# Kernel optimization log

Measured on AMD Instinct MI355X. Metric: run time of the kernel, lower is better.

The kernel has to match this reference:

```python
import jax, jax.numpy as jnp
import numpy as np
from jax import lax


def setup_inputs() -> dict:
    key = jax.random.key(0)
    k1, k2 = jax.random.split(key)
    B, C, H, W = 4, 64, 64, 64
    foreground = jax.random.normal(k1, (B, C, H, W), dtype=jnp.float32)
    masks = jax.random.uniform(k2, (B, 1, H, W), dtype=jnp.float32)
    return {"foreground": foreground, "masks": masks}


def reference(foreground, masks):
    # First-call path of KnowledgeConsistentAttention (att_scores_prev is None).
    # patch_size=3 -> padding=1 around 1x1 dynamic kernels; propagate_size=3 -> 3x3 sum pool.
    B, C, H, W = foreground.shape
    P = H * W
    # Dynamic 1x1 kernels: one per spatial location, L2-normalized over channels.
    K = foreground.reshape(B, C, P).transpose(0, 2, 1)            # [B, P, C]
    norm = jnp.sqrt(jnp.sum(K * K, axis=2, keepdims=True))        # flatten(1).norm per kernel
    K = K / (norm + 1e-8)
    # conv2d with 1x1 kernels and padding=1 == GEMM over zero-padded input.
    Xpad = jnp.pad(foreground, ((0, 0), (0, 0), (1, 1), (1, 1)))  # [B, C, H+2, W+2]
    scores = jnp.einsum('bpc,bchw->bphw', K, Xpad)                # [B, P, H+2, W+2]
    # avg_pool2d(k=3, stride=1, pad=1) * 9 == zero-padded 3x3 sum pool.
    scores = lax.reduce_window(scores, jnp.float32(0.0), lax.add,
                               (1, 1, 3, 3), (1, 1, 1, 1), 'SAME')
    attn = jax.nn.softmax(scores, axis=1)                          # softmax over P kernels
    # conv_transpose2d with 1x1 kernels, padding=1 crops the border back to HxW.
    out = jnp.einsum('bphw,bpc->bchw', attn[:, :, 1:-1, 1:-1], K)  # [B, C, H, W]
    return out
```

## Files before the change

kernel.cpp:

```cpp
#include <hip/hip_runtime.h>
#include <hip/hip_bf16.h>
#include <math.h>

#define Bn 4
#define Cn 64
#define Pn 4096
#define QT 32
#define PBK 128
#define NITER (Pn / PBK)
#define LOG2E 1.4426950408889634f

typedef __attribute__((ext_vector_type(8))) short short8;
typedef __attribute__((ext_vector_type(4))) short short4v;
typedef __attribute__((ext_vector_type(4))) float float4v;
typedef unsigned short bfu;

__device__ __forceinline__ bfu f2bf(float x) {
    unsigned u = __float_as_uint(x);
    u = (u + 0x7fffu + ((u >> 16) & 1u)) >> 16;
    return (bfu)u;
}

__device__ __forceinline__ void async_load16(const bfu* g, bfu* l) {
    __builtin_amdgcn_global_load_lds(
        (const __attribute__((address_space(1))) unsigned int*)(const void*)g,
        (__attribute__((address_space(3))) unsigned int*)(void*)l,
        16, 0, 0);
}

__global__ __launch_bounds__(256) void prep_kernel(const float* __restrict__ fg,
                                                   bfu* __restrict__ Kpc,
                                                   bfu* __restrict__ Kcp2,
                                                   float* __restrict__ S) {
    __shared__ float shbuf[64 * 64];
    int t = threadIdx.x;
    if (blockIdx.x < 512) {
        float* tile  = shbuf;
        float* rnorm = shbuf + 64 * 33;
        int b  = blockIdx.x >> 7;
        int p0 = (blockIdx.x & 127) << 5;
        const float* src = fg + (size_t)b * Cn * Pn + p0;
        #pragma unroll
        for (int i = 0; i < 8; ++i) {
            int idx = i * 256 + t;
            int c = idx >> 5, p = idx & 31;
            tile[c * 33 + p] = src[(size_t)c * Pn + p];
        }
        __syncthreads();
        if (t < 32) {
            float ss = 0.f;
            #pragma unroll
            for (int c = 0; c < 64; ++c) { float v = tile[c * 33 + t]; ss += v * v; }
            rnorm[t] = 1.0f / (sqrtf(ss) + 1e-8f);
        }
        __syncthreads();
        bfu* dpc = Kpc + ((size_t)b * Pn + p0) * Cn;
        #pragma unroll
        for (int i = 0; i < 8; ++i) {
            int idx = i * 256 + t;
            int p = idx >> 6, c = idx & 63;
            dpc[(size_t)p * Cn + c] = f2bf(tile[c * 33 + p] * rnorm[p]);
        }
        bfu* d2 = Kcp2 + ((size_t)b * 256 + (p0 >> 4)) * 1024;
        #pragma unroll
        for (int i = 0; i < 8; ++i) {
            int idx = i * 256 + t;
            int c = idx >> 5, p = idx & 31;
            d2[(size_t)(p >> 4) * 1024 + c * 16 + (p & 15)] =
                f2bf(tile[c * 33 + p] * rnorm[p]);
        }
    } else {
        float (*pl)[64] = (float(*)[64])shbuf;
        int bc = blockIdx.x - 512;
        const float* src = fg + (size_t)bc * Pn;
        float*       dst = S  + (size_t)bc * Pn;
        #pragma unroll
        for (int i = 0; i < 16; ++i) {
            int idx = i * 256 + t;
            pl[idx >> 6][idx & 63] = src[idx];
        }
        __syncthreads();
        #pragma unroll
        for (int i = 0; i < 16; ++i) {
            int idx = i * 256 + t;
            int h = idx >> 6, w = idx & 63;
            float s = 0.f;
            #pragma unroll
            for (int dh = -1; dh <= 1; ++dh) {
                int hh = h + dh;
                if (hh < 0 || hh >= 64) continue;
                #pragma unroll
                for (int dw = -1; dw <= 1; ++dw) {
                    int ww = w + dw;
                    if (ww < 0 || ww >= 64) continue;
                    s += pl[hh][ww];
                }
            }
            dst[idx] = s * LOG2E;
        }
    }
}

__global__ __launch_bounds__(512, 4) void flash_kernel(const bfu* __restrict__ Kpc,
                                                       const bfu* __restrict__ Kcp2,
                                                       const float* __restrict__ S,
                                                       float* __restrict__ out) {
    __shared__ __align__(16) bfu smem[18432];
    __shared__ float wredl[8][QT];
    bfu* Sl = smem + 16384;

    int b  = blockIdx.x >> 7;
    int q0 = (blockIdx.x & 127) * QT;
    int t  = threadIdx.x;
    int w = t >> 6, l = t & 63, lq = l & 15, quad = l >> 4;

    const float* Sg  = S    + (size_t)b * Cn * Pn;
    const bfu*   gpc = Kpc  + (size_t)b * Pn * Cn;
    const bfu*   gt  = Kcp2 + (size_t)b * 256 * 1024;

    {
        int c = t >> 3, qq = (t & 7) * 4;
        const float* sp = &Sg[(size_t)c * Pn + q0 + qq];
        float4 v0 = *(const float4*)sp;
        float vv[4] = {v0.x, v0.y, v0.z, v0.w};
        int ch = c >> 3, cl = c & 7;
        #pragma unroll
        for (int i = 0; i < 4; ++i) {
            int row = qq + i;
            Sl[row * 64 + ((ch ^ (row & 7)) << 3) + cl] = f2bf(vv[i]);
        }
    }

    {
        const bfu* src = gt + (size_t)w * 1024 + l * 8;
        bfu* dst = smem + w * 1024;
        async_load16(src, dst);
        async_load16(src + 512, dst + 512);
    }
    __syncthreads();

    short8 bs[2][2];
    #pragma unroll
    for (int nt = 0; nt < 2; ++nt)
        #pragma unroll
        for (int ks = 0; ks < 2; ++ks) {
            int row = nt * 16 + lq;
            bs[nt][ks] = *(const short8*)&Sl[row * 64 + (((ks * 4 + quad) ^ (lq & 7)) << 3)];
        }

    float4v o[2][4];
    #pragma unroll
    for (int nt = 0; nt < 2; ++nt)
        #pragma unroll
        for (int cb = 0; cb < 4; ++cb) o[nt][cb] = (float4v){0.f, 0.f, 0.f, 0.f};
    float lacc[2] = {0.f, 0.f};

    for (int pb = 0; pb < NITER; ++pb) {
        bfu* tile = smem + (pb & 1) * 8192 + w * 1024;

        const bfu* ap = gpc + ((size_t)pb * PBK + 16 * w + lq) * Cn + quad * 8;
        float4 a0 = *(const float4*)ap;
        float4 a1 = *(const float4*)(ap + 32);

        if (pb + 1 < NITER) {
            const bfu* src = gt + ((size_t)(pb + 1) * 8 + w) * 1024 + l * 8;
            bfu* dst = smem + ((pb + 1) & 1) * 8192 + w * 1024;
            async_load16(src, dst);
            async_load16(src + 512, dst + 512);
        }

        short8 af0 = *(short8*)&a0, af1 = *(short8*)&a1;
        float4v sc[2];
        #pragma unroll
        for (int nt = 0; nt < 2; ++nt) {
            float4v acc = (float4v){0.f, 0.f, 0.f, 0.f};
            acc = __builtin_amdgcn_mfma_f32_16x16x32_bf16(af0, bs[nt][0], acc, 0, 0, 0);
            acc = __builtin_amdgcn_mfma_f32_16x16x32_bf16(af1, bs[nt][1], acc, 0, 0, 0);
            sc[nt] = acc;
        }

        short4v epk[2];
        #pragma unroll
        for (int nt = 0; nt < 2; ++nt) {
            float e0 = __builtin_amdgcn_exp2f(sc[nt][0]);
            float e1 = __builtin_amdgcn_exp2f(sc[nt][1]);
            float e2 = __builtin_amdgcn_exp2f(sc[nt][2]);
            float e3 = __builtin_amdgcn_exp2f(sc[nt][3]);
            lacc[nt] += (e0 + e1) + (e2 + e3);
            short4v ep = {(short)f2bf(e0), (short)f2bf(e1), (short)f2bf(e2), (short)f2bf(e3)};
            epk[nt] = ep;
        }

        __builtin_amdgcn_s_waitcnt(0x0F72);
        __builtin_amdgcn_sched_barrier(0);

        #pragma unroll
        for (int cb = 0; cb < 4; ++cb) {
            short4v kb = *(const short4v*)&tile[(16 * cb + lq) * 16 + quad * 4];
            o[0][cb] = __builtin_amdgcn_mfma_f32_16x16x16bf16_1k(epk[0], kb, o[0][cb], 0, 0, 0);
            o[1][cb] = __builtin_amdgcn_mfma_f32_16x16x16bf16_1k(epk[1], kb, o[1][cb], 0, 0, 0);
        }
    }

    #pragma unroll
    for (int nt = 0; nt < 2; ++nt) {
        lacc[nt] += __shfl_xor(lacc[nt], 16);
        lacc[nt] += __shfl_xor(lacc[nt], 32);
    }
    if (quad == 0) { wredl[w][lq] = lacc[0]; wredl[w][16 + lq] = lacc[1]; }

    float* Ol = (float*)smem;
    __syncthreads();
    if (w < 4) {
        #pragma unroll
        for (int nt = 0; nt < 2; ++nt)
            #pragma unroll
            for (int cb = 0; cb < 4; ++cb)
                #pragma unroll
                for (int r = 0; r < 4; ++r)
                    Ol[(w * 32 + nt * 16 + quad * 4 + r) * 66 + cb * 16 + lq] = o[nt][cb][r];
    }
    __syncthreads();
    if (w >= 4) {
        #pragma unroll
        for (int nt = 0; nt < 2; ++nt)
            #pragma unroll
            for (int cb = 0; cb < 4; ++cb)
                #pragma unroll
                for (int r = 0; r < 4; ++r)
                    Ol[((w - 4) * 32 + nt * 16 + quad * 4 + r) * 66 + cb * 16 + lq] += o[nt][cb][r];
    }
    __syncthreads();

    float* og = out + (size_t)b * Cn * Pn;
    #pragma unroll
    for (int i = 0; i < 4; ++i) {
        int idx = i * 512 + t;
        int c = idx >> 5, q = idx & 31;
        float lsum = ((wredl[0][q] + wredl[1][q]) + (wredl[2][q] + wredl[3][q])) +
                     ((wredl[4][q] + wredl[5][q]) + (wredl[6][q] + wredl[7][q]));
        float v = ((Ol[q * 66 + c] + Ol[(32 + q) * 66 + c]) +
                   (Ol[(64 + q) * 66 + c] + Ol[(96 + q) * 66 + c])) / lsum;
        og[(size_t)c * Pn + q0 + q] = v;
    }
}

extern "C" void kernel_launch(void* const* d_in, const int* in_sizes, int n_in,
                              void* d_out, int out_size, void* d_ws, size_t ws_size,
                              hipStream_t stream) {
    const float* fg = (const float*)d_in[0];
    float* out = (float*)d_out;
    bfu*   Kpc  = (bfu*)d_ws;
    bfu*   Kcp2 = Kpc + (size_t)Bn * Pn * Cn;
    float* S    = (float*)(Kcp2 + (size_t)Bn * Pn * Cn);

    prep_kernel <<<768, 256, 0, stream>>>(fg, Kpc, Kcp2, S);
    flash_kernel<<<Bn * 128, 512, 0, stream>>>(Kpc, Kcp2, S, out);
}
```

Before: 105.8 us.

## Double query tile per block to halve K streaming and grid size

Increases the query tile from 32 to 64 columns per block, so each block carries twice as many score/output MFMA tiles and reuses every streamed K tile across more queries. The grid shrinks to one block per CU with remapped batch/tile indexing, and the epilogue reduction layout is transposed. This is meant to cut redundant global/L2 traffic for K, at the cost of higher register and LDS use and lower occupancy for hiding latency.

New measurement: 95.98 us. 9.3% less time.

```diff
diff --git a/kernel.cpp b/kernel.cpp
--- a/kernel.cpp
+++ b/kernel.cpp
@@ -5,7 +5,7 @@
 #define Bn 4
 #define Cn 64
 #define Pn 4096
-#define QT 32
+#define QT 64
 #define PBK 128
 #define NITER (Pn / PBK)
 #define LOG2E 1.4426950408889634f
@@ -101,16 +101,18 @@
     }
 }
 
-__global__ __launch_bounds__(512, 4) void flash_kernel(const bfu* __restrict__ Kpc,
+__global__ __launch_bounds__(512, 1) void flash_kernel(const bfu* __restrict__ Kpc,
                                                        const bfu* __restrict__ Kcp2,
                                                        const float* __restrict__ S,
                                                        float* __restrict__ out) {
-    __shared__ __align__(16) bfu smem[18432];
+    __shared__ __align__(16) bfu smem[33792];
     __shared__ float wredl[8][QT];
     bfu* Sl = smem + 16384;
 
-    int b  = blockIdx.x >> 7;
-    int q0 = (blockIdx.x & 127) * QT;
+    int i  = blockIdx.x;
+    int b  = (i & 7) >> 1;
+    int qt = ((i >> 3) << 1) | (i & 1);
+    int q0 = qt * QT;
     int t  = threadIdx.x;
     int w = t >> 6, l = t & 63, lq = l & 15, quad = l >> 4;
 
@@ -119,15 +121,16 @@
     const bfu*   gt  = Kcp2 + (size_t)b * 256 * 1024;
 
     {
-        int c = t >> 3, qq = (t & 7) * 4;
+        int c = t >> 3, qq = (t & 7) * 8;
         const float* sp = &Sg[(size_t)c * Pn + q0 + qq];
         float4 v0 = *(const float4*)sp;
-        float vv[4] = {v0.x, v0.y, v0.z, v0.w};
+        float4 v1 = *(const float4*)(sp + 4);
+        float vv[8] = {v0.x, v0.y, v0.z, v0.w, v1.x, v1.y, v1.z, v1.w};
         int ch = c >> 3, cl = c & 7;
         #pragma unroll
-        for (int i = 0; i < 4; ++i) {
-            int row = qq + i;
-            Sl[row * 64 + ((ch ^ (row & 7)) << 3) + cl] = f2bf(vv[i]);
+        for (int k = 0; k < 8; ++k) {
+            int row = qq + k;
+            Sl[row * 64 + ((ch ^ (row & 7)) << 3) + cl] = f2bf(vv[k]);
         }
     }
 
@@ -139,21 +142,21 @@
     }
     __syncthreads();
 
-    short8 bs[2][2];
-    #pragma unroll
-    for (int nt = 0; nt < 2; ++nt)
+    short8 bs[4][2];
+    #pragma unroll
+    for (int nt = 0; nt < 4; ++nt)
         #pragma unroll
         for (int ks = 0; ks < 2; ++ks) {
             int row = nt * 16 + lq;
             bs[nt][ks] = *(const short8*)&Sl[row * 64 + (((ks * 4 + quad) ^ (lq & 7)) << 3)];
         }
 
-    float4v o[2][4];
-    #pragma unroll
-    for (int nt = 0; nt < 2; ++nt)
+    float4v o[4][4];
+    #pragma unroll
+    for (int nt = 0; nt < 4; ++nt)
         #pragma unroll
         for (int cb = 0; cb < 4; ++cb) o[nt][cb] = (float4v){0.f, 0.f, 0.f, 0.f};
-    float lacc[2] = {0.f, 0.f};
+    float lacc[4] = {0.f, 0.f, 0.f, 0.f};
 
     for (int pb = 0; pb < NITER; ++pb) {
         bfu* tile = smem + (pb & 1) * 8192 + w * 1024;
@@ -170,18 +173,18 @@
         }
 
         short8 af0 = *(short8*)&a0, af1 = *(short8*)&a1;
-        float4v sc[2];
-        #pragma unroll
-        for (int nt = 0; nt < 2; ++nt) {
+        float4v sc[4];
+        #pragma unroll
+        for (int nt = 0; nt < 4; ++nt) {
             float4v acc = (float4v){0.f, 0.f, 0.f, 0.f};
             acc = __builtin_amdgcn_mfma_f32_16x16x32_bf16(af0, bs[nt][0], acc, 0, 0, 0);
             acc = __builtin_amdgcn_mfma_f32_16x16x32_bf16(af1, bs[nt][1], acc, 0, 0, 0);
             sc[nt] = acc;
         }
 
-        short4v epk[2];
-        #pragma unroll
-        for (int nt = 0; nt < 2; ++nt) {
+        short4v epk[4];
+        #pragma unroll
+        for (int nt = 0; nt < 4; ++nt) {
             float e0 = __builtin_amdgcn_exp2f(sc[nt][0]);
             float e1 = __builtin_amdgcn_exp2f(sc[nt][1]);
             float e2 = __builtin_amdgcn_exp2f(sc[nt][2]);
@@ -197,50 +200,53 @@
         #pragma unroll
         for (int cb = 0; cb < 4; ++cb) {
             short4v kb = *(const short4v*)&tile[(16 * cb + lq) * 16 + quad * 4];
-            o[0][cb] = __builtin_amdgcn_mfma_f32_16x16x16bf16_1k(epk[0], kb, o[0][cb], 0, 0, 0);
-            o[1][cb] = __builtin_amdgcn_mfma_f32_16x16x16bf16_1k(epk[1], kb, o[1][cb], 0, 0, 0);
-        }
-    }
-
-    #pragma unroll
-    for (int nt = 0; nt < 2; ++nt) {
+            #pragma unroll
+            for (int nt = 0; nt < 4; ++nt)
+                o[nt][cb] = __builtin_amdgcn_mfma_f32_16x16x16bf16_1k(epk[nt], kb, o[nt][cb], 0, 0, 0);
+        }
+    }
+
+    #pragma unroll
+    for (int nt = 0; nt < 4; ++nt) {
         lacc[nt] += __shfl_xor(lacc[nt], 16);
         lacc[nt] += __shfl_xor(lacc[nt], 32);
     }
-    if (quad == 0) { wredl[w][lq] = lacc[0]; wredl[w][16 + lq] = lacc[1]; }
+    if (quad == 0)
+        #pragma unroll
+        for (int nt = 0; nt < 4; ++nt) wredl[w][nt * 16 + lq] = lacc[nt];
 
     float* Ol = (float*)smem;
     __syncthreads();
     if (w < 4) {
         #pragma unroll
-        for (int nt = 0; nt < 2; ++nt)
+        for (int nt = 0; nt < 4; ++nt)
             #pragma unroll
             for (int cb = 0; cb < 4; ++cb)
                 #pragma unroll
                 for (int r = 0; r < 4; ++r)
-                    Ol[(w * 32 + nt * 16 + quad * 4 + r) * 66 + cb * 16 + lq] = o[nt][cb][r];
+                    Ol[(w * 64 + 16 * cb + lq) * 66 + nt * 16 + quad * 4 + r] = o[nt][cb][r];
     }
     __syncthreads();
     if (w >= 4) {
         #pragma unroll
-        for (int nt = 0; nt < 2; ++nt)
+        for (int nt = 0; nt < 4; ++nt)
             #pragma unroll
             for (int cb = 0; cb < 4; ++cb)
                 #pragma unroll
                 for (int r = 0; r < 4; ++r)
-                    Ol[((w - 4) * 32 + nt * 16 + quad * 4 + r) * 66 + cb * 16 + lq] += o[nt][cb][r];
+                    Ol[((w - 4) * 64 + 16 * cb + lq) * 66 + nt * 16 + quad * 4 + r] += o[nt][cb][r];
     }
     __syncthreads();
 
     float* og = out + (size_t)b * Cn * Pn;
     #pragma unroll
-    for (int i = 0; i < 4; ++i) {
-        int idx = i * 512 + t;
-        int c = idx >> 5, q = idx & 31;
+    for (int k = 0; k < 8; ++k) {
+        int idx = k * 512 + t;
+        int c = idx >> 6, q = idx & 63;
         float lsum = ((wredl[0][q] + wredl[1][q]) + (wredl[2][q] + wredl[3][q])) +
                      ((wredl[4][q] + wredl[5][q]) + (wredl[6][q] + wredl[7][q]));
-        float v = ((Ol[q * 66 + c] + Ol[(32 + q) * 66 + c]) +
-                   (Ol[(64 + q) * 66 + c] + Ol[(96 + q) * 66 + c])) / lsum;
+        float v = ((Ol[c * 66 + q] + Ol[(64 + c) * 66 + q]) +
+                   (Ol[(128 + c) * 66 + q] + Ol[(192 + c) * 66 + q])) / lsum;
         og[(size_t)c * Pn + q0 + q] = v;
     }
 }
@@ -255,5 +261,5 @@
     float* S    = (float*)(Kcp2 + (size_t)Bn * Pn * Cn);
 
     prep_kernel <<<768, 256, 0, stream>>>(fg, Kpc, Kcp2, S);
-    flash_kernel<<<Bn * 128, 512, 0, stream>>>(Kpc, Kcp2, S, out);
-}
+    flash_kernel<<<Bn * 64, 512, 0, stream>>>(Kpc, Kcp2, S, out);
+}
```
